# Kernel optimization log

Measured on AMD Instinct MI355X. Metric: run time of the kernel, lower is better.

Reference implementation:

```python
import jax, jax.numpy as jnp
import numpy as np

NEG_SLOPE = 0.2  # GATConv default negative_slope

def setup_inputs() -> dict:
    key = jax.random.key(0)
    k1, k2, k3, k4 = jax.random.split(key, 4)
    N, Cin, Cout = 2048, 128, 64
    return {
        "data": jax.random.normal(k1, (N, Cin), jnp.float32),
        "W": jax.random.normal(k2, (Cin, Cout), jnp.float32) / np.sqrt(Cin).astype(np.float32),
        "att_src": jax.random.normal(k3, (Cout,), jnp.float32) * 0.1,
        "att_dst": jax.random.normal(k4, (Cout,), jnp.float32) * 0.1,
        "bias": jnp.zeros((Cout,), jnp.float32),
    }

def reference(data, W, att_src, att_dst, bias):
    N = data.shape[0]
    # torch.combinations(arange(N)).t(): edges (i, j) with i < j, src=i, dst=j
    rows, cols = jnp.triu_indices(N, k=1)
    loop = jnp.arange(N)  # GATConv add_self_loops=True
    src = jnp.concatenate([rows, loop])
    dst = jnp.concatenate([cols, loop])

    h = data @ W                       # [N, Cout]
    a_s = h @ att_src                  # [N]
    a_d = h @ att_dst                  # [N]

    # per-edge attention logits, leaky_relu, segment softmax over dst
    e = jax.nn.leaky_relu(a_s[src] + a_d[dst], NEG_SLOPE)          # [E]
    m = jax.ops.segment_max(e, dst, num_segments=N)                # [N]
    ex = jnp.exp(e - m[dst])                                       # [E]
    denom = jax.ops.segment_sum(ex, dst, num_segments=N)           # [N]
    alpha = ex / denom[dst]                                        # [E]

    # scatter-add weighted source features
    out = jax.ops.segment_sum(alpha[:, None] * h[src], dst, num_segments=N) + bias
    return jax.nn.relu(out)
```

## Files before the change

kernel.cpp:

```cpp
#include <hip/hip_runtime.h>
#include <hip/hip_bf16.h>
#include <math.h>

#define N 2048
#define CIN 128
#define COUT 64
#define NEG 0.2f
#define JB 16
#define NJB (N / JB)

typedef __attribute__((ext_vector_type(8))) short short8;
typedef __attribute__((ext_vector_type(4))) float f32x4;

__device__ __forceinline__ ushort bf16u(float x) {
  __hip_bfloat16 b = __float2bfloat16(x);
  return *reinterpret_cast<ushort*>(&b);
}
__device__ __forceinline__ uint pack2(float lo, float hi) {
  return (uint)bf16u(lo) | ((uint)bf16u(hi) << 16);
}

__global__ __launch_bounds__(256) void gat_gemm_mfma(
    const float* __restrict__ data, const float* __restrict__ W,
    const float* __restrict__ att_src, const float* __restrict__ att_dst,
    ushort* __restrict__ hfrag, float* __restrict__ a_s,
    float* __restrict__ a_d) {
  const int tid = (int)threadIdx.x;
  const int ci = tid >> 6;
  const int lane = tid & 63;
  const int i0 = (int)blockIdx.x * 16;
  const int q = lane >> 4;
  const int n15 = lane & 15;
  const int mrow = i0 + n15;

  short8 af[4];
#pragma unroll
  for (int kc = 0; kc < 4; ++kc) {
    const int col = kc * 32 + q * 8;
    const float4 f0 = *(const float4*)&data[mrow * CIN + col];
    const float4 f1 = *(const float4*)&data[mrow * CIN + col + 4];
    uint4 pa;
    pa.x = pack2(f0.x, f0.y);
    pa.y = pack2(f0.z, f0.w);
    pa.z = pack2(f1.x, f1.y);
    pa.w = pack2(f1.z, f1.w);
    af[kc] = *(short8*)&pa;
  }

  const int cg = ci * 16 + n15;
  f32x4 acc = {0.f, 0.f, 0.f, 0.f};
#pragma unroll
  for (int kc = 0; kc < 4; ++kc) {
    const int kr = kc * 32 + q * 8;
    ushort uw[8];
#pragma unroll
    for (int e = 0; e < 8; ++e) uw[e] = bf16u(W[(kr + e) * COUT + cg]);
    uint4 pw;
    pw.x = (uint)uw[0] | ((uint)uw[1] << 16);
    pw.y = (uint)uw[2] | ((uint)uw[3] << 16);
    pw.z = (uint)uw[4] | ((uint)uw[5] << 16);
    pw.w = (uint)uw[6] | ((uint)uw[7] << 16);
    acc = __builtin_amdgcn_mfma_f32_16x16x32_bf16(af[kc], *(short8*)&pw,
                                                  acc, 0, 0, 0);
  }

  {
    const int ib = i0 + q * 4;
    const int f = (ib >> 5) * 4 + ci;
    const int lp = ((ib >> 3) & 3) * 16 + n15;
    uint2 hv;
    hv.x = pack2(acc[0], acc[1]);
    hv.y = pack2(acc[2], acc[3]);
    *(uint2*)&hfrag[((size_t)(f * 64 + lp) << 3) + (ib & 7)] = hv;
  }

  __shared__ float asp[4][16];
  __shared__ float adp[4][16];
  {
    const float sc = att_src[cg];
    const float dc = att_dst[cg];
    float ps[4], pd[4];
#pragma unroll
    for (int r = 0; r < 4; ++r) { ps[r] = acc[r] * sc; pd[r] = acc[r] * dc; }
#pragma unroll
    for (int off = 1; off < 16; off <<= 1) {
#pragma unroll
      for (int r = 0; r < 4; ++r) {
        ps[r] += __shfl_xor(ps[r], off);
        pd[r] += __shfl_xor(pd[r], off);
      }
    }
    if (n15 == 0) {
#pragma unroll
      for (int r = 0; r < 4; ++r) {
        asp[ci][q * 4 + r] = ps[r];
        adp[ci][q * 4 + r] = pd[r];
      }
    }
  }
  __syncthreads();
  if (tid < 16) {
    a_s[i0 + tid] = asp[0][tid] + asp[1][tid] + asp[2][tid] + asp[3][tid];
    a_d[i0 + tid] = adp[0][tid] + adp[1][tid] + adp[2][tid] + adp[3][tid];
  }
}

__global__ __launch_bounds__(1024) void gat_attn_flash(
    const ushort* __restrict__ hfrag, const float* __restrict__ a_s,
    const float* __restrict__ a_d, const float* __restrict__ bias,
    float* __restrict__ out) {
  const int bj = NJB - 1 - (int)blockIdx.x;
  const int tid = (int)threadIdx.x;
  const int wid = tid >> 6;
  const int lane = tid & 63;
  const int j0 = bj * JB;
  const int jme = j0 + (lane & 15);
  const int kgrp = lane >> 4;
  const float ad_me = a_d[jme];
  const int nks = (bj + 2) >> 1;

  f32x4 acc0 = {0.f, 0.f, 0.f, 0.f};
  f32x4 acc1 = acc0, acc2 = acc0, acc3 = acc0;
  float dsum = 0.f;
  const uint4* hf = (const uint4*)hfrag;

  for (int ks = wid; ks < nks; ks += 16) {
    const int ibase = ks * 32 + kgrp * 8;
    const float4 asa = *(const float4*)&a_s[ibase];
    const float4 asb = *(const float4*)&a_s[ibase + 4];
    const float av[8] = {asa.x, asa.y, asa.z, asa.w,
                         asb.x, asb.y, asb.z, asb.w};
    short8 afw;
#pragma unroll
    for (int e = 0; e < 8; ++e) {
      float x = av[e] + ad_me;
      x = fmaxf(x, NEG * x);
      float wgt = __expf(x);
      if (ibase + e > jme) wgt = 0.f;
      dsum += wgt;
      afw[e] = (short)bf16u(wgt);
    }
    const int fbase = (ks * 4) * 64 + lane;
    const uint4 b0 = hf[fbase];
    const uint4 b1 = hf[fbase + 64];
    const uint4 b2 = hf[fbase + 128];
    const uint4 b3 = hf[fbase + 192];
    acc0 = __builtin_amdgcn_mfma_f32_16x16x32_bf16(afw, *(const short8*)&b0,
                                                   acc0, 0, 0, 0);
    acc1 = __builtin_amdgcn_mfma_f32_16x16x32_bf16(afw, *(const short8*)&b1,
                                                   acc1, 0, 0, 0);
    acc2 = __builtin_amdgcn_mfma_f32_16x16x32_bf16(afw, *(const short8*)&b2,
                                                   acc2, 0, 0, 0);
    acc3 = __builtin_amdgcn_mfma_f32_16x16x32_bf16(afw, *(const short8*)&b3,
                                                   acc3, 0, 0, 0);
  }

  dsum += __shfl_xor(dsum, 16);
  dsum += __shfl_xor(dsum, 32);

  __shared__ float rbuf[16][16][64];
  __shared__ float dbuf[16][16];
#pragma unroll
  for (int r = 0; r < 4; ++r) {
    rbuf[0 + r][wid][lane]  = acc0[r];
    rbuf[4 + r][wid][lane]  = acc1[r];
    rbuf[8 + r][wid][lane]  = acc2[r];
    rbuf[12 + r][wid][lane] = acc3[r];
  }
  if (lane < 16) dbuf[wid][lane] = dsum;
  __syncthreads();

  {
    const int j = tid >> 6, c = tid & 63;
    const int qq = j >> 2, rr = j & 3, t16 = c >> 4, n = c & 15;
    float num = 0.f, den = 0.f;
#pragma unroll
    for (int ww = 0; ww < 16; ++ww) {
      num += rbuf[t16 * 4 + rr][ww][qq * 16 + n];
      den += dbuf[ww][j];
    }
    const float v = num / den + bias[c];
    out[(size_t)(j0 + j) * COUT + c] = v > 0.f ? v : 0.f;
  }
}

extern "C" void kernel_launch(void* const* d_in, const int* in_sizes, int n_in,
                              void* d_out, int out_size, void* d_ws, size_t ws_size,
                              hipStream_t stream) {
  const float* data    = (const float*)d_in[0];
  const float* W       = (const float*)d_in[1];
  const float* att_src = (const float*)d_in[2];
  const float* att_dst = (const float*)d_in[3];
  const float* bias    = (const float*)d_in[4];
  float* out = (float*)d_out;

  ushort* hfrag = (ushort*)d_ws;
  float* a_s  = (float*)d_ws + 65536;
  float* a_d  = a_s + N;

  gat_gemm_mfma<<<N / 16, 256, 0, stream>>>(data, W, att_src, att_dst,
                                            hfrag, a_s, a_d);
  gat_attn_flash<<<NJB, 1024, 0, stream>>>(hfrag, a_s, a_d, bias, out);
}
```

Before: 15.45 us.

## Split attention kernel across output channel halves to double block count

Each attention block now handles only half of the 64 output channels, and the grid is doubled to 256 blocks. This raises parallelism on a GPU with many CUs, since 128 blocks left many CUs idle. It also shrinks the shared-memory reduction buffer. The cost is that the exp/leaky-relu weight computation and the a_s loads are now done twice, once per channel half.

```diff
diff --git a/kernel.cpp b/kernel.cpp
--- a/kernel.cpp
+++ b/kernel.cpp
@@ -109,7 +109,9 @@
     const ushort* __restrict__ hfrag, const float* __restrict__ a_s,
     const float* __restrict__ a_d, const float* __restrict__ bias,
     float* __restrict__ out) {
-  const int bj = NJB - 1 - (int)blockIdx.x;
+  const int b = (int)blockIdx.x;
+  const int bj = NJB - 1 - (b >> 1);
+  const int chalf = b & 1;
   const int tid = (int)threadIdx.x;
   const int wid = tid >> 6;
   const int lane = tid & 63;
@@ -120,7 +122,7 @@
   const int nks = (bj + 2) >> 1;
 
   f32x4 acc0 = {0.f, 0.f, 0.f, 0.f};
-  f32x4 acc1 = acc0, acc2 = acc0, acc3 = acc0;
+  f32x4 acc1 = acc0;
   float dsum = 0.f;
   const uint4* hf = (const uint4*)hfrag;
 
@@ -140,47 +142,40 @@
       dsum += wgt;
       afw[e] = (short)bf16u(wgt);
     }
-    const int fbase = (ks * 4) * 64 + lane;
+    const int fbase = (ks * 4 + chalf * 2) * 64 + lane;
     const uint4 b0 = hf[fbase];
     const uint4 b1 = hf[fbase + 64];
-    const uint4 b2 = hf[fbase + 128];
-    const uint4 b3 = hf[fbase + 192];
     acc0 = __builtin_amdgcn_mfma_f32_16x16x32_bf16(afw, *(const short8*)&b0,
                                                    acc0, 0, 0, 0);
     acc1 = __builtin_amdgcn_mfma_f32_16x16x32_bf16(afw, *(const short8*)&b1,
                                                    acc1, 0, 0, 0);
-    acc2 = __builtin_amdgcn_mfma_f32_16x16x32_bf16(afw, *(const short8*)&b2,
-                                                   acc2, 0, 0, 0);
-    acc3 = __builtin_amdgcn_mfma_f32_16x16x32_bf16(afw, *(const short8*)&b3,
-                                                   acc3, 0, 0, 0);
   }
 
   dsum += __shfl_xor(dsum, 16);
   dsum += __shfl_xor(dsum, 32);
 
-  __shared__ float rbuf[16][16][64];
+  __shared__ float rbuf[8][16][64];
   __shared__ float dbuf[16][16];
 #pragma unroll
   for (int r = 0; r < 4; ++r) {
-    rbuf[0 + r][wid][lane]  = acc0[r];
-    rbuf[4 + r][wid][lane]  = acc1[r];
-    rbuf[8 + r][wid][lane]  = acc2[r];
-    rbuf[12 + r][wid][lane] = acc3[r];
+    rbuf[r][wid][lane]     = acc0[r];
+    rbuf[4 + r][wid][lane] = acc1[r];
   }
   if (lane < 16) dbuf[wid][lane] = dsum;
   __syncthreads();
 
-  {
-    const int j = tid >> 6, c = tid & 63;
-    const int qq = j >> 2, rr = j & 3, t16 = c >> 4, n = c & 15;
+  if (tid < 512) {
+    const int j = tid >> 5, cl = tid & 31;
+    const int qq = j >> 2, rr = j & 3, t16 = cl >> 4, n = cl & 15;
     float num = 0.f, den = 0.f;
 #pragma unroll
     for (int ww = 0; ww < 16; ++ww) {
       num += rbuf[t16 * 4 + rr][ww][qq * 16 + n];
       den += dbuf[ww][j];
     }
-    const float v = num / den + bias[c];
-    out[(size_t)(j0 + j) * COUT + c] = v > 0.f ? v : 0.f;
+    const int cg = chalf * 32 + cl;
+    const float v = num / den + bias[cg];
+    out[(size_t)(j0 + j) * COUT + cg] = v > 0.f ? v : 0.f;
   }
 }
 
@@ -200,5 +195,5 @@
 
   gat_gemm_mfma<<<N / 16, 256, 0, stream>>>(data, W, att_src, att_dst,
                                             hfrag, a_s, a_d);
-  gat_attn_flash<<<NJB, 1024, 0, stream>>>(hfrag, a_s, a_d, bias, out);
+  gat_attn_flash<<<NJB * 2, 1024, 0, stream>>>(hfrag, a_s, a_d, bias, out);
 }
```

After: 14.44 us (median of 2 runs). 1.07x faster.
